# Optimization experiments

Hardware: AMD Instinct MI355X
Metric: run time of the kernel (lower is better)

Reference implementation:

```python
import jax, jax.numpy as jnp
import numpy as np

KSIZE = 5
PAD = 2  # replicate padding per side for 'same' 5x5x5 box filter


def setup_inputs() -> dict:
    key = jax.random.key(0)
    # mp: [N, C, D, H, W] nonnegative probability maps
    mp = jax.random.uniform(key, (1, 21, 16, 256, 256), dtype=jnp.float32)
    return {"mp": mp}


def reference(mp):
    N, C, D, H, W = mp.shape
    # replicate ('edge') padding on D, H, W, then depthwise 5x5x5 box filter
    x = jnp.pad(mp, ((0, 0), (0, 0), (PAD, PAD), (PAD, PAD), (PAD, PAD)), mode="edge")
    k = jnp.full((C, 1, KSIZE, KSIZE, KSIZE), 1.0 / (KSIZE ** 3), dtype=mp.dtype)
    y = jax.lax.conv_general_dilated(
        x, k,
        window_strides=(1, 1, 1),
        padding="VALID",
        dimension_numbers=("NCDHW", "OIDHW", "NCDHW"),
        feature_group_count=C,
    )  # [N, C, D, H, W]

    # normalize over channel axis (torch permutes to put channels first; we keep axis=1)
    y = y / jnp.sum(y, axis=1, keepdims=True)

    # weighted-median selection: running cumulative sum over channels
    s = jnp.cumsum(y, axis=1)                     # [N, C, D, H, W]
    idx = jnp.arange(C).reshape(1, C, 1, 1, 1)    # channel indices

    # med0: LAST channel i with y[i] > 0 and cumsum < 0.5 (torch loop overwrites), default 0
    med0 = jnp.maximum(
        jnp.max(jnp.where((y > 0) & (s < 0.5), idx, -1), axis=1, keepdims=True), 0
    )
    # med1: torch sets med[1] only while med[1]==0, so the result is the FIRST
    # NONZERO channel with cumsum > 0.5 (i=0 qualifying leaves med[1]==0 and gets
    # overwritten by the next qualifying i); 0 if no nonzero channel qualifies.
    med1 = jnp.argmax((s > 0.5) & (idx > 0), axis=1, keepdims=True)

    keep = (idx == med0) | (idx == med1)
    return jnp.where(keep, y, jnp.zeros((), dtype=y.dtype))
```

## Files before the change

### kernel.cpp

```cpp
#include <hip/hip_runtime.h>

#define CC   21
#define DD   16
#define HH   256
#define WW   256
#define HWP  (HH * WW)
#define DHW  (DD * HWP)

typedef float f4a __attribute__((ext_vector_type(4), aligned(16)));
__device__ __forceinline__ f4a f4add(f4a a, f4a b) { return a + b; }

#define GLDS16(gp, lp)                                                        \
    __builtin_amdgcn_global_load_lds(                                         \
        (const __attribute__((address_space(1))) void*)(gp),                  \
        (__attribute__((address_space(3))) void*)(lp), 16, 0, 0)

#define A_SZ (DD * PYN_ * 32)
#define PYN_ 12

#define NB1  (8 * 32 * CC)
#define CHK1 (NB1 / 8)

__global__ __launch_bounds__(256, 5) void dh_blur_kernel(const float* __restrict__ mp,
                                                         float* __restrict__ out) {
    __shared__ float A[DD * PYN_ * 32];
    const int tid = threadIdx.x;

    const int bid = blockIdx.x;
    const int t   = (bid & 7) * CHK1 + (bid >> 3);
    const int yb  = t & 31;
    const int wt  = (t >> 5) & 7;
    const int ch  = t >> 8;
    const int w0  = wt * 32;
    const int h0  = yb * 8;
    const float* __restrict__ src = mp + (size_t)ch * DHW + w0;

    {
        const int wv   = tid >> 6;
        const int lane = tid & 63;
#pragma unroll
        for (int j = 0; j < 6; ++j) {
            const int inst = wv * 6 + j;
            const int idx4 = inst * 64 + lane;
            const int d    = idx4 / 96;
            const int r    = idx4 - d * 96;
            const int py   = r >> 3;
            const int x4   = r & 7;
            const int h    = min(HH - 1, max(0, h0 + py - 2));
            const float* gp = src + (size_t)d * HWP + (size_t)h * WW + x4 * 4;
            GLDS16(gp, &A[inst * 256]);
        }
    }
    __syncthreads();

    if (tid < 96) {
        const int py = tid >> 3;
        const int x4 = tid & 7;
        float* colA = &A[py * 32 + x4 * 4];

        f4a P[16];
#pragma unroll
        for (int d = 0; d < 16; ++d) P[d] = *(const f4a*)(colA + d * 384);

        constexpr int M0[12] = {0, 0, 0, 1, 2, 3, 4, 5, 6, 7, 8, 9};
        constexpr int M1[12] = {6, 7, 8, 9, 10, 11, 12, 13, 14, 15, 15, 15};

        {
            f4a sum = f4add(f4add(f4add(P[M0[0]], P[M0[1]]),
                                  f4add(P[M0[2]], P[M0[3]])), P[M0[4]]);
#pragma unroll
            for (int i = 0; i < 8; ++i) {
                *(f4a*)(colA + i * 384) = sum;
                if (i < 7) sum = sum - P[M0[i]] + P[M0[i + 5]];
            }
        }
        {
            f4a sum = f4add(f4add(f4add(P[M1[0]], P[M1[1]]),
                                  f4add(P[M1[2]], P[M1[3]])), P[M1[4]]);
#pragma unroll
            for (int i = 0; i < 8; ++i) {
                *(f4a*)(colA + (8 + i) * 384) = sum;
                if (i < 7) sum = sum - P[M1[i]] + P[M1[i + 5]];
            }
        }
    }
    __syncthreads();

#pragma unroll
    for (int it = 0; it < 4; ++it) {
        const int tt   = tid + it * 256;
        const int xx4  = tt & 7;
        const int y    = (tt >> 3) & 7;
        const int dout = tt >> 6;

        const float* b = &A[dout * 384 + y * 32 + xx4 * 4];
        f4a a = *(const f4a*)b;
#pragma unroll
        for (int k = 1; k < 5; ++k) a = f4add(a, *(const f4a*)(b + k * 32));

        *(f4a*)(out + (size_t)ch * DHW + (size_t)dout * HWP
                + (size_t)(h0 + y) * WW + w0 + xx4 * 4) = a;
    }
}

#define ROWP 264

__global__ __launch_bounds__(256) void wmedian_kernel(float* __restrict__ y4) {
    __shared__ float R[CC * ROWP];

    const int h = blockIdx.x;
    const int d = blockIdx.y;
    const int tid = threadIdx.x;
    float* __restrict__ base = y4 + (size_t)d * HWP + (size_t)h * WW;

    for (int idx = tid; idx < CC * 64; idx += 256) {
        const int c  = idx >> 6;
        const int w4 = idx & 63;
        *(f4a*)(&R[c * ROWP + 4 + w4 * 4]) = *(const f4a*)(base + (size_t)c * DHW + w4 * 4);
    }
    if (tid < CC) {
        const float v0 = base[(size_t)tid * DHW];
        const float vL = base[(size_t)tid * DHW + (WW - 1)];
        R[tid * ROWP + 2]   = v0;
        R[tid * ROWP + 3]   = v0;
        R[tid * ROWP + 260] = vL;
        R[tid * ROWP + 261] = vL;
    }
    __syncthreads();

    const int w = tid;
    float v[CC];
    float tot = 0.f;
#pragma unroll
    for (int c = 0; c < CC; ++c) {
        const float* r = &R[c * ROWP + 2 + w];
        v[c] = ((((r[0] + r[1]) + r[2]) + r[3]) + r[4]);
        tot += v[c];
    }
    const float inv = 1.0f / tot;

    float s = 0.f, sv0 = 0.f, sv1 = 0.f;
    int m0 = 0, m1 = 0;
#pragma unroll
    for (int c = 0; c < CC; ++c) {
        const float yn = v[c] * inv;
        const float sn = s + yn;
        if (c == 0) { sv0 = yn; sv1 = yn; }
        if (v[c] > 0.f && sn < 0.5f) { m0 = c; sv0 = yn; }
        if (m1 == 0 && c > 0 && sn > 0.5f) { m1 = c; sv1 = yn; }
        s = sn;
    }

#pragma unroll
    for (int c = 0; c < CC; ++c) {
        base[(size_t)c * DHW + w] = (c == m0) ? sv0 : ((c == m1) ? sv1 : 0.f);
    }
}

extern "C" void kernel_launch(void* const* d_in, const int* in_sizes, int n_in,
                              void* d_out, int out_size, void* d_ws, size_t ws_size,
                              hipStream_t stream) {
    const float* mp = (const float*)d_in[0];
    float* out = (float*)d_out;

    dh_blur_kernel<<<NB1, 256, 0, stream>>>(mp, out);
    wmedian_kernel<<<dim3(HH, DD), 256, 0, stream>>>(out);
}
```

Measured before the change: 185.4 us.

## Make blur kernel persistent with double-buffered LDS tile prefetch

Turns the depth/height blur kernel into a persistent kernel: 768 blocks each process 7 tiles, and the LDS is double-buffered so the global-to-LDS loads for the next tile are issued while the current tile is computed and stored. This is meant to hide load latency and cut per-block launch and staging overhead. In exchange LDS use doubles and occupancy is lowered to 3 blocks per CU. Correctness depends on hand-placed s_waitcnt counts, for example vmcnt(4) to let the output stores drain while the next tile's loads are still pending.

```diff
diff --git a/kernel.cpp b/kernel.cpp
--- a/kernel.cpp
+++ b/kernel.cpp
@@ -15,91 +15,110 @@
         (const __attribute__((address_space(1))) void*)(gp),                  \
         (__attribute__((address_space(3))) void*)(lp), 16, 0, 0)
 
-#define A_SZ (DD * PYN_ * 32)
-#define PYN_ 12
+#define TILE_WORDS (DD * 12 * 32)
+#define NB1   768
+#define TPB   7
 
-#define NB1  (8 * 32 * CC)
-#define CHK1 (NB1 / 8)
+__device__ __forceinline__ void stage_tile(const float* __restrict__ mp,
+                                           float* __restrict__ buf,
+                                           int t, int wv, int lane) {
+    const int yb = t & 31;
+    const int wt = (t >> 5) & 7;
+    const int ch = t >> 8;
+    const int h0 = yb * 8;
+    const float* __restrict__ src = mp + (size_t)ch * DHW + wt * 32;
+#pragma unroll
+    for (int j = 0; j < 6; ++j) {
+        const int inst = wv * 6 + j;
+        const int idx4 = inst * 64 + lane;
+        const int d    = idx4 / 96;
+        const int r    = idx4 - d * 96;
+        const int py   = r >> 3;
+        const int x4   = r & 7;
+        const int h    = min(HH - 1, max(0, h0 + py - 2));
+        GLDS16(src + (size_t)d * HWP + (size_t)h * WW + x4 * 4, buf + inst * 256);
+    }
+}
 
-__global__ __launch_bounds__(256, 5) void dh_blur_kernel(const float* __restrict__ mp,
+__global__ __launch_bounds__(256, 3) void dh_blur_kernel(const float* __restrict__ mp,
                                                          float* __restrict__ out) {
-    __shared__ float A[DD * PYN_ * 32];
-    const int tid = threadIdx.x;
+    __shared__ float A[2 * TILE_WORDS];
+    const int tid  = threadIdx.x;
+    const int wv   = tid >> 6;
+    const int lane = tid & 63;
 
-    const int bid = blockIdx.x;
-    const int t   = (bid & 7) * CHK1 + (bid >> 3);
-    const int yb  = t & 31;
-    const int wt  = (t >> 5) & 7;
-    const int ch  = t >> 8;
-    const int w0  = wt * 32;
-    const int h0  = yb * 8;
-    const float* __restrict__ src = mp + (size_t)ch * DHW + w0;
+    const int xcd  = blockIdx.x & 7;
+    const int slot = blockIdx.x >> 3;
+    const int tbase = xcd * 672 + slot;
 
-    {
-        const int wv   = tid >> 6;
-        const int lane = tid & 63;
+    stage_tile(mp, A, tbase, wv, lane);
+    asm volatile("s_waitcnt vmcnt(0)" ::: "memory");
+    __builtin_amdgcn_s_barrier();
+
+    for (int it = 0; it < TPB; ++it) {
+        const int t  = tbase + it * 96;
+        const int yb = t & 31;
+        const int wt = (t >> 5) & 7;
+        const int ch = t >> 8;
+        const int w0 = wt * 32;
+        const int h0 = yb * 8;
+        float* const cur = A + (it & 1) * TILE_WORDS;
+        float* const nxt = A + ((it & 1) ^ 1) * TILE_WORDS;
+
+        if (it + 1 < TPB) stage_tile(mp, nxt, tbase + (it + 1) * 96, wv, lane);
+
+        if (tid < 96) {
+            const int py = tid >> 3;
+            const int x4 = tid & 7;
+            float* colA = cur + py * 32 + x4 * 4;
+
+            f4a P[16];
 #pragma unroll
-        for (int j = 0; j < 6; ++j) {
-            const int inst = wv * 6 + j;
-            const int idx4 = inst * 64 + lane;
-            const int d    = idx4 / 96;
-            const int r    = idx4 - d * 96;
-            const int py   = r >> 3;
-            const int x4   = r & 7;
-            const int h    = min(HH - 1, max(0, h0 + py - 2));
-            const float* gp = src + (size_t)d * HWP + (size_t)h * WW + x4 * 4;
-            GLDS16(gp, &A[inst * 256]);
-        }
-    }
-    __syncthreads();
+            for (int d = 0; d < 16; ++d) P[d] = *(const f4a*)(colA + d * 384);
 
-    if (tid < 96) {
-        const int py = tid >> 3;
-        const int x4 = tid & 7;
-        float* colA = &A[py * 32 + x4 * 4];
+            constexpr int M0[12] = {0, 0, 0, 1, 2, 3, 4, 5, 6, 7, 8, 9};
+            constexpr int M1[12] = {6, 7, 8, 9, 10, 11, 12, 13, 14, 15, 15, 15};
 
-        f4a P[16];
+            {
+                f4a sum = f4add(f4add(f4add(P[M0[0]], P[M0[1]]),
+                                      f4add(P[M0[2]], P[M0[3]])), P[M0[4]]);
 #pragma unroll
-        for (int d = 0; d < 16; ++d) P[d] = *(const f4a*)(colA + d * 384);
-
-        constexpr int M0[12] = {0, 0, 0, 1, 2, 3, 4, 5, 6, 7, 8, 9};
-        constexpr int M1[12] = {6, 7, 8, 9, 10, 11, 12, 13, 14, 15, 15, 15};
-
-        {
-            f4a sum = f4add(f4add(f4add(P[M0[0]], P[M0[1]]),
-                                  f4add(P[M0[2]], P[M0[3]])), P[M0[4]]);
+                for (int i = 0; i < 8; ++i) {
+                    *(f4a*)(colA + i * 384) = sum;
+                    if (i < 7) sum = sum - P[M0[i]] + P[M0[i + 5]];
+                }
+            }
+            {
+                f4a sum = f4add(f4add(f4add(P[M1[0]], P[M1[1]]),
+                                      f4add(P[M1[2]], P[M1[3]])), P[M1[4]]);
 #pragma unroll
-            for (int i = 0; i < 8; ++i) {
-                *(f4a*)(colA + i * 384) = sum;
-                if (i < 7) sum = sum - P[M0[i]] + P[M0[i + 5]];
+                for (int i = 0; i < 8; ++i) {
+                    *(f4a*)(colA + (8 + i) * 384) = sum;
+                    if (i < 7) sum = sum - P[M1[i]] + P[M1[i + 5]];
+                }
             }
         }
-        {
-            f4a sum = f4add(f4add(f4add(P[M1[0]], P[M1[1]]),
-                                  f4add(P[M1[2]], P[M1[3]])), P[M1[4]]);
-#pragma unroll
-            for (int i = 0; i < 8; ++i) {
-                *(f4a*)(colA + (8 + i) * 384) = sum;
-                if (i < 7) sum = sum - P[M1[i]] + P[M1[i + 5]];
-            }
-        }
-    }
-    __syncthreads();
+        asm volatile("s_waitcnt lgkmcnt(0)" ::: "memory");
+        __builtin_amdgcn_s_barrier();
 
 #pragma unroll
-    for (int it = 0; it < 4; ++it) {
-        const int tt   = tid + it * 256;
-        const int xx4  = tt & 7;
-        const int y    = (tt >> 3) & 7;
-        const int dout = tt >> 6;
+        for (int it2 = 0; it2 < 4; ++it2) {
+            const int tt   = tid + it2 * 256;
+            const int xx4  = tt & 7;
+            const int y    = (tt >> 3) & 7;
+            const int dout = tt >> 6;
 
-        const float* b = &A[dout * 384 + y * 32 + xx4 * 4];
-        f4a a = *(const f4a*)b;
+            const float* b = cur + dout * 384 + y * 32 + xx4 * 4;
+            f4a a = *(const f4a*)b;
 #pragma unroll
-        for (int k = 1; k < 5; ++k) a = f4add(a, *(const f4a*)(b + k * 32));
+            for (int k = 1; k < 5; ++k) a = f4add(a, *(const f4a*)(b + k * 32));
 
-        *(f4a*)(out + (size_t)ch * DHW + (size_t)dout * HWP
-                + (size_t)(h0 + y) * WW + w0 + xx4 * 4) = a;
+            *(f4a*)(out + (size_t)ch * DHW + (size_t)dout * HWP
+                    + (size_t)(h0 + y) * WW + w0 + xx4 * 4) = a;
+        }
+
+        asm volatile("s_waitcnt vmcnt(4)" ::: "memory");
+        __builtin_amdgcn_s_barrier();
     }
 }
 
```

Measured after the change: 186.6 us. No clear change (+0.6%).
